# Performance work log

Hardware: AMD Instinct MI355X
Metric: run time of the kernel (lower is better)

The kernel has to match this reference:

```python
import jax, jax.numpy as jnp
import numpy as np

SPACE_DIM = 3
D = SPACE_DIM + 1            # (t, x, y, z)
D_MODEL = 1024
N_LAYERS = 4                 # hidden layers
N_MIX = 64
TRI = D * (D - 1) // 2       # strict upper-triangular entries of A
OUT_DIM = N_MIX * (TRI + 1)  # per-mixture triu values + mixture logits
TRIU_I, TRIU_J = np.triu_indices(D, k=1)
RHO_SCALE = 10.0


def setup_inputs() -> dict:
    key = jax.random.key(0)
    ks = jax.random.split(key, 8)
    B = 65536
    x = jax.random.normal(ks[0], (B, D), jnp.float32)
    W0 = jax.random.normal(ks[1], (D, D_MODEL), jnp.float32) * np.float32(np.sqrt(2.0 / D))
    b0 = jnp.zeros((D_MODEL,), jnp.float32)
    Wh = jax.random.normal(ks[2], (N_LAYERS, D_MODEL, D_MODEL), jnp.float32) * np.float32(np.sqrt(2.0 / D_MODEL))
    bh = jnp.zeros((N_LAYERS, D_MODEL), jnp.float32)
    Wout = jax.random.normal(ks[3], (D_MODEL, OUT_DIM), jnp.float32) * np.float32(np.sqrt(1.0 / D_MODEL))
    bout = jnp.zeros((OUT_DIM,), jnp.float32)
    return dict(x=x, W0=W0, b0=b0, Wh=Wh, bh=bh, Wout=Wout, bout=bout)


def _mlp(z, W0, b0, Wh, bh, Wout, bout):
    # z: (D,) -> (OUT_DIM,), swish MLP (NeuralConservationLaw backbone)
    h = jax.nn.silu(z @ W0 + b0)
    for l in range(N_LAYERS):  # fixed small layer count: python loop ok
        h = jax.nn.silu(h @ Wh[l] + bh[l])
    return h @ Wout + bout


def _A(z, params):
    # Antisymmetric matrix field A(z): mixture-weighted strict-upper-tri values.
    out = _mlp(z, *params)                              # (OUT_DIM,)
    logits = out[:N_MIX]                                # (N_MIX,)
    vals = out[N_MIX:].reshape(N_MIX, TRI)              # (N_MIX, TRI)
    a = jax.nn.softmax(logits) @ vals                   # (TRI,)
    A = jnp.zeros((D, D), out.dtype).at[TRIU_I, TRIU_J].set(a)
    return A - A.T                                      # antisymmetric (D, D)


def reference(x, W0, b0, Wh, bh, Wout, bout):
    params = (W0, b0, Wh, bh, Wout, bout)

    def u_single(z):
        # u_i = sum_j dA_ij/dz_j  (row-divergence of antisymmetric A => div u = 0)
        J = jax.jacfwd(lambda zz: _A(zz, params))(z)    # (D, D, D): J[i,j,k]=dA_ij/dz_k
        return jnp.einsum('ijj->i', J)                  # (D,)

    u = jax.vmap(u_single)(x)                           # (B, D)
    rho = u[..., :1] * RHO_SCALE
    flux = u[..., 1:]
    return jnp.concatenate([rho, flux], axis=-1)
```

## Files before the change

### kernel.cpp

```cpp
#include <hip/hip_runtime.h>
#include <hip/hip_bf16.h>

typedef _Float16 half8 __attribute__((ext_vector_type(8)));
typedef _Float16 half4 __attribute__((ext_vector_type(4)));
typedef float floatx4 __attribute__((ext_vector_type(4)));

__device__ __forceinline__ float bfu2f(unsigned short u) {
  return __uint_as_float(((unsigned)u) << 16);
}

__device__ __forceinline__ void gld16(const void* g, void* l) {
  __builtin_amdgcn_global_load_lds((const __attribute__((address_space(1))) void*)g,
                                   (__attribute__((address_space(3))) void*)l, 16, 0, 0);
}

__device__ __forceinline__ float fast_sig(float v) {
  return __builtin_amdgcn_rcpf(1.f + __expf(-v));
}

template <int NC>
__device__ __forceinline__ void xcd_decode(int lin, int NR, int& r, int& c) {
  if (NR & 7) {
    c = lin % NC;
    r = lin / NC;
  } else {
    int rl = lin & 7;
    int t = lin >> 3;
    c = t % NC;
    r = (t / NC) * 8 + rl;
  }
}

__global__ void probe_kernel(const unsigned short* __restrict__ w0, int* __restrict__ flag) {
  __shared__ int s;
  if (threadIdx.x == 0) s = 0;
  __syncthreads();
  int big = 0;
  for (int i = threadIdx.x; i < 2048; i += 256) {
    unsigned e = (w0[i] >> 7) & 0xFFu;
    if (e >= 134u) big = 1;
  }
  if (big) atomicOr(&s, 1);
  __syncthreads();
  if (threadIdx.x == 0) *flag = s;
}

__global__ void cvt_kernel(const void* __restrict__ in, _Float16* __restrict__ out, int nOut,
                           int nIn, const int* __restrict__ flag) {
  int i = blockIdx.x * 256 + threadIdx.x;
  if (i >= nOut) return;
  float v = 0.f;
  if (i < nIn) v = (*flag) ? ((const float*)in)[i] : bfu2f(((const unsigned short*)in)[i]);
  out[i] = (_Float16)v;
}

__global__ void tr_kernel(const void* __restrict__ in, _Float16* __restrict__ out, int Nin,
                          long inStride, long outStride, const int* __restrict__ flag) {
  __shared__ float tile[32][33];
  const int f = *flag;
  int k0 = blockIdx.x * 32, n0 = blockIdx.y * 32;
  long ib = (long)blockIdx.z * inStride;
  long ob = (long)blockIdx.z * outStride;
  int tx = threadIdx.x, ty = threadIdx.y;
#pragma unroll
  for (int i = 0; i < 4; i++) {
    int k = k0 + ty + i * 8, n = n0 + tx;
    float v = 0.f;
    if (n < Nin) {
      long idx = ib + (long)k * Nin + n;
      v = f ? ((const float*)in)[idx] : bfu2f(((const unsigned short*)in)[idx]);
    }
    tile[ty + i * 8][tx] = v;
  }
  __syncthreads();
#pragma unroll
  for (int i = 0; i < 4; i++) {
    int n = n0 + ty + i * 8, k = k0 + tx;
    out[ob + (long)n * 1024 + k] = (_Float16)tile[tx][ty + i * 8];
  }
}

__global__ __launch_bounds__(256)
void layer0_kernel(const _Float16* __restrict__ x16, const _Float16* __restrict__ W0c,
                   const _Float16* __restrict__ b0c, _Float16* __restrict__ H,
                   int chunkBase, int S1) {
  const int lb = blockIdx.x;
  const int t = threadIdx.x;
  const long gb = (long)chunkBase + lb;
  float z0 = (float)x16[gb * 4 + 0];
  float z1 = (float)x16[gb * 4 + 1];
  float z2 = (float)x16[gb * 4 + 2];
  float z3 = (float)x16[gb * 4 + 3];
  const int j0 = t * 4;
  float w[4][4];
#pragma unroll
  for (int i = 0; i < 4; i++) {
    half4 wv = *(const half4*)&W0c[i * 1024 + j0];
#pragma unroll
    for (int jj = 0; jj < 4; jj++) w[i][jj] = (float)wv[jj];
  }
  half4 o[5];
#pragma unroll
  for (int jj = 0; jj < 4; jj++) {
    float pre = z0 * w[0][jj] + z1 * w[1][jj] + z2 * w[2][jj] + z3 * w[3][jj] +
                (float)b0c[j0 + jj];
    float s = fast_sig(pre);
    o[0][jj] = (_Float16)(pre * s);
    float ds = s * (1.f + pre * (1.f - s));
    o[1][jj] = (_Float16)(ds * w[0][jj]);
    o[2][jj] = (_Float16)(ds * w[1][jj]);
    o[3][jj] = (_Float16)(ds * w[2][jj]);
    o[4][jj] = (_Float16)(ds * w[3][jj]);
  }
  long rowbase = (long)lb * 1024 + j0;
#pragma unroll
  for (int s = 0; s < 5; s++) *(half4*)&H[(long)s * S1 + rowbase] = o[s];
}

__global__ __launch_bounds__(256, 3)
void gemm_h1(const _Float16* __restrict__ A, const _Float16* __restrict__ Bt,
             const _Float16* __restrict__ bias, _Float16* __restrict__ C,
             _Float16* __restrict__ DS, int NR) {
  constexpr int K = 1024;
  __shared__ _Float16 SM[8192];
  _Float16* As = SM;
  _Float16* Bs = SM + 4096;
  _Float16* Ep = SM;
  const int tid = threadIdx.x;
  const int wave = tid >> 6;
  const int lane = tid & 63;
  int rb, cb;
  xcd_decode<8>(blockIdx.x, NR, rb, cb);
  const int n0 = cb * 128;
  const long m0 = (long)rb * 128;

  const int srow0 = (wave * 2 + 0) * 16 + (lane >> 2);
  const int srow1 = (wave * 2 + 1) * 16 + (lane >> 2);
  const int scol = (lane & 3) * 8;
  const _Float16* gA0 = A + (m0 + srow0) * K + scol;
  const _Float16* gA1 = A + (m0 + srow1) * K + scol;
  const _Float16* gB0 = Bt + (long)(n0 + srow0) * K + scol;
  const _Float16* gB1 = Bt + (long)(n0 + srow1) * K + scol;
  _Float16* lA0 = As + (wave * 2 + 0) * 512;
  _Float16* lA1 = As + (wave * 2 + 1) * 512;
  _Float16* lB0 = Bs + (wave * 2 + 0) * 512;
  _Float16* lB1 = Bs + (wave * 2 + 1) * 512;

  const int wm = (wave & 1) * 64;
  const int wn = (wave >> 1) * 64;
  const int fr = lane & 15;
  const int fc = (lane >> 4) * 8;
  const int c0f = lane & 15;
  const int rqk = lane >> 4;
  const int myRound = wave & 1;

  float bv[4];
#pragma unroll
  for (int ni = 0; ni < 4; ni++) bv[ni] = (float)bias[n0 + wn + ni * 16 + c0f];

  const int erow = tid >> 4;
  const int ecol = (tid & 15) * 8;
  const int ecolp = ecol ^ (wave << 4);

  floatx4 acc[4][4];
#pragma unroll
  for (int i = 0; i < 4; i++)
#pragma unroll
    for (int j = 0; j < 4; j++) acc[i][j] = (floatx4)(0.f);

  for (int kk = 0; kk < K; kk += 32) {
    __syncthreads();
    gld16(gA0 + kk, lA0);
    gld16(gA1 + kk, lA1);
    gld16(gB0 + kk, lB0);
    gld16(gB1 + kk, lB1);
    __syncthreads();
    half8 af[4], bf[4];
#pragma unroll
    for (int i = 0; i < 4; i++) af[i] = *(const half8*)&As[(wm + i * 16 + fr) * 32 + fc];
#pragma unroll
    for (int i = 0; i < 4; i++) bf[i] = *(const half8*)&Bs[(wn + i * 16 + fr) * 32 + fc];
#pragma unroll
    for (int mi = 0; mi < 4; mi++)
#pragma unroll
      for (int ni = 0; ni < 4; ni++)
        acc[mi][ni] = __builtin_amdgcn_mfma_f32_16x16x32_f16(af[mi], bf[ni], acc[mi][ni], 0, 0, 0);
  }

#pragma unroll
  for (int r = 0; r < 2; r++) {
    __syncthreads();
    if (myRound == r) {
#pragma unroll
      for (int mi = 0; mi < 4; mi++)
#pragma unroll
        for (int ni = 0; ni < 4; ni++) {
          int colp = (wn + ni * 16 + c0f) ^ (rqk << 4);
#pragma unroll
          for (int rr = 0; rr < 4; rr++) {
            int row_local = mi * 16 + rqk * 4 + rr;
            Ep[row_local * 128 + colp] = (_Float16)(acc[mi][ni][rr] + bv[ni]);
          }
        }
    }
    __syncthreads();
#pragma unroll
    for (int p = 0; p < 4; p++) {
      int row_local = p * 16 + erow;
      half8 vv = *(const half8*)&Ep[row_local * 128 + ecolp];
      long row = m0 + r * 64 + row_local;
      half8 hv, dv;
#pragma unroll
      for (int e = 0; e < 8; e++) {
        float xv = (float)vv[e];
        float sg = fast_sig(xv);
        hv[e] = (_Float16)(xv * sg);
        dv[e] = (_Float16)(sg * (1.f + xv * (1.f - sg)));
      }
      *(half8*)&C[row * (long)K + n0 + ecol] = hv;
      *(half8*)&DS[row * (long)K + n0 + ecol] = dv;
    }
  }
}

__global__ __launch_bounds__(256, 4)
void gemm_h2(const _Float16* __restrict__ A, const _Float16* __restrict__ Bt,
             _Float16* __restrict__ C, const _Float16* __restrict__ DS, int bcMask, int NR) {
  constexpr int K = 1024;
  __shared__ _Float16 SM[8192];
  _Float16* As = SM;
  _Float16* Bs = SM + 4096;
  _Float16* Ep = SM;
  const int tid = threadIdx.x;
  const int wave = tid >> 6;
  const int lane = tid & 63;
  int rb, cb;
  xcd_decode<8>(blockIdx.x, NR, rb, cb);
  const int n0 = cb * 128;
  const long m0 = (long)rb * 128;

  const int srow0 = (wave * 2 + 0) * 16 + (lane >> 2);
  const int srow1 = (wave * 2 + 1) * 16 + (lane >> 2);
  const int scol = (lane & 3) * 8;
  const _Float16* gA0 = A + (m0 + srow0) * K + scol;
  const _Float16* gA1 = A + (m0 + srow1) * K + scol;
  const _Float16* gB0 = Bt + (long)(n0 + srow0) * K + scol;
  const _Float16* gB1 = Bt + (long)(n0 + srow1) * K + scol;
  _Float16* lA0 = As + (wave * 2 + 0) * 512;
  _Float16* lA1 = As + (wave * 2 + 1) * 512;
  _Float16* lB0 = Bs + (wave * 2 + 0) * 512;
  _Float16* lB1 = Bs + (wave * 2 + 1) * 512;

  const int wm = (wave & 1) * 64;
  const int wn = (wave >> 1) * 64;
  const int fr = lane & 15;
  const int fc = (lane >> 4) * 8;
  const int c0f = lane & 15;
  const int rqk = lane >> 4;
  const int myRound = wave & 1;

  const int erow = tid >> 4;
  const int ecol = (tid & 15) * 8;
  const int ecolp = ecol ^ (wave << 4);

  floatx4 acc[4][4];
#pragma unroll
  for (int i = 0; i < 4; i++)
#pragma unroll
    for (int j = 0; j < 4; j++) acc[i][j] = (floatx4)(0.f);

  for (int kk = 0; kk < K; kk += 32) {
    __syncthreads();
    gld16(gA0 + kk, lA0);
    gld16(gA1 + kk, lA1);
    gld16(gB0 + kk, lB0);
    gld16(gB1 + kk, lB1);
    __syncthreads();
    half8 af[4], bf[4];
#pragma unroll
    for (int i = 0; i < 4; i++) af[i] = *(const half8*)&As[(wm + i * 16 + fr) * 32 + fc];
#pragma unroll
    for (int i = 0; i < 4; i++) bf[i] = *(const half8*)&Bs[(wn + i * 16 + fr) * 32 + fc];
#pragma unroll
    for (int mi = 0; mi < 4; mi++)
#pragma unroll
      for (int ni = 0; ni < 4; ni++)
        acc[mi][ni] = __builtin_amdgcn_mfma_f32_16x16x32_f16(af[mi], bf[ni], acc[mi][ni], 0, 0, 0);
  }

#pragma unroll
  for (int r = 0; r < 2; r++) {
    __syncthreads();
    if (myRound == r) {
#pragma unroll
      for (int mi = 0; mi < 4; mi++)
#pragma unroll
        for (int ni = 0; ni < 4; ni++) {
          int colp = (wn + ni * 16 + c0f) ^ (rqk << 4);
#pragma unroll
          for (int rr = 0; rr < 4; rr++) {
            int row_local = mi * 16 + rqk * 4 + rr;
            Ep[row_local * 128 + colp] = (_Float16)acc[mi][ni][rr];
          }
        }
    }
    __syncthreads();
#pragma unroll
    for (int p = 0; p < 4; p++) {
      int row_local = p * 16 + erow;
      half8 vv = *(const half8*)&Ep[row_local * 128 + ecolp];
      long row = m0 + r * 64 + row_local;
      half8 dv = *(const half8*)&DS[(long)(row & bcMask) * K + n0 + ecol];
      *(half8*)&C[row * (long)K + n0 + ecol] = dv * vv;
    }
  }
}

__global__ __launch_bounds__(256, 4)
void gemm_out(const _Float16* __restrict__ A, const _Float16* __restrict__ Bt,
              const _Float16* __restrict__ bias, _Float16* __restrict__ C,
              int Nreal, int ldc, int biasRows, int NR) {
  constexpr int K = 1024;
  __shared__ _Float16 SM[8192];
  _Float16* As = SM;
  _Float16* Bs = SM + 4096;
  _Float16* Ep = SM;
  const int tid = threadIdx.x;
  const int wave = tid >> 6;
  const int lane = tid & 63;
  int rb, cb;
  xcd_decode<4>(blockIdx.x, NR, rb, cb);
  const int n0 = cb * 128;
  const long m0 = (long)rb * 128;

  const int srow0 = (wave * 2 + 0) * 16 + (lane >> 2);
  const int srow1 = (wave * 2 + 1) * 16 + (lane >> 2);
  const int scol = (lane & 3) * 8;
  const _Float16* gA0 = A + (m0 + srow0) * K + scol;
  const _Float16* gA1 = A + (m0 + srow1) * K + scol;
  const _Float16* gB0 = Bt + (long)(n0 + srow0) * K + scol;
  const _Float16* gB1 = Bt + (long)(n0 + srow1) * K + scol;
  _Float16* lA0 = As + (wave * 2 + 0) * 512;
  _Float16* lA1 = As + (wave * 2 + 1) * 512;
  _Float16* lB0 = Bs + (wave * 2 + 0) * 512;
  _Float16* lB1 = Bs + (wave * 2 + 1) * 512;

  const int wm = (wave & 1) * 64;
  const int wn = (wave >> 1) * 64;
  const int fr = lane & 15;
  const int fc = (lane >> 4) * 8;
  const int c0f = lane & 15;
  const int rqk = lane >> 4;
  const int myRound = wave & 1;

  float bv[4];
#pragma unroll
  for (int ni = 0; ni < 4; ni++) bv[ni] = (float)bias[n0 + wn + ni * 16 + c0f];

  const int erow = tid >> 4;
  const int ecol = (tid & 15) * 8;
  const int ecolp = ecol ^ (wave << 4);

  floatx4 acc[4][4];
#pragma unroll
  for (int i = 0; i < 4; i++)
#pragma unroll
    for (int j = 0; j < 4; j++) acc[i][j] = (floatx4)(0.f);

  for (int kk = 0; kk < K; kk += 32) {
    __syncthreads();
    gld16(gA0 + kk, lA0);
    gld16(gA1 + kk, lA1);
    gld16(gB0 + kk, lB0);
    gld16(gB1 + kk, lB1);
    __syncthreads();
    half8 af[4], bf[4];
#pragma unroll
    for (int i = 0; i < 4; i++) af[i] = *(const half8*)&As[(wm + i * 16 + fr) * 32 + fc];
#pragma unroll
    for (int i = 0; i < 4; i++) bf[i] = *(const half8*)&Bs[(wn + i * 16 + fr) * 32 + fc];
#pragma unroll
    for (int mi = 0; mi < 4; mi++)
#pragma unroll
      for (int ni = 0; ni < 4; ni++)
        acc[mi][ni] = __builtin_amdgcn_mfma_f32_16x16x32_f16(af[mi], bf[ni], acc[mi][ni], 0, 0, 0);
  }

#pragma unroll
  for (int r = 0; r < 2; r++) {
    __syncthreads();
    if (myRound == r) {
#pragma unroll
      for (int mi = 0; mi < 4; mi++)
#pragma unroll
        for (int ni = 0; ni < 4; ni++) {
          int colp = (wn + ni * 16 + c0f) ^ (rqk << 4);
#pragma unroll
          for (int rr = 0; rr < 4; rr++) {
            int row_local = mi * 16 + rqk * 4 + rr;
            long grow = m0 + wm + mi * 16 + rqk * 4 + rr;
            float v = acc[mi][ni][rr] + (grow < biasRows ? bv[ni] : 0.f);
            Ep[row_local * 128 + colp] = (_Float16)v;
          }
        }
    }
    __syncthreads();
#pragma unroll
    for (int p = 0; p < 4; p++) {
      int row_local = p * 16 + erow;
      int col = n0 + ecol;
      if (col < Nreal) {
        half8 vv = *(const half8*)&Ep[row_local * 128 + ecolp];
        long row = m0 + r * 64 + row_local;
        *(half8*)&C[row * (long)ldc + col] = vv;
      }
    }
  }
}

__global__ __launch_bounds__(256)
void finalize_kernel(const _Float16* __restrict__ O5, void* __restrict__ outp,
                     int chunkBase, int Bc, const int* __restrict__ flag) {
  const int wid = threadIdx.x >> 6;
  const int lane = threadIdx.x & 63;
  const int lb = blockIdx.x * 4 + wid;
  const long SO = (long)Bc * 448;
  const long base0 = (long)lb * 448;

  union UU { unsigned u; _Float16 h[2]; };

  float lg = (float)O5[base0 + lane];
  float vals[6];
  {
    const unsigned* vp = (const unsigned*)(O5 + base0 + 64 + lane * 6);
#pragma unroll
    for (int q = 0; q < 3; q++) {
      UU c; c.u = vp[q];
      vals[2 * q] = (float)c.h[0];
      vals[2 * q + 1] = (float)c.h[1];
    }
  }
  float dl[4], dv[4][6];
#pragma unroll
  for (int t = 0; t < 4; t++) {
    long bs = (long)(1 + t) * SO + base0;
    dl[t] = (float)O5[bs + lane];
    const unsigned* vp = (const unsigned*)(O5 + bs + 64 + lane * 6);
#pragma unroll
    for (int q = 0; q < 3; q++) {
      UU c; c.u = vp[q];
      dv[t][2 * q] = (float)c.h[0];
      dv[t][2 * q + 1] = (float)c.h[1];
    }
  }
  float mx = lg;
#pragma unroll
  for (int off = 32; off >= 1; off >>= 1) mx = fmaxf(mx, __shfl_xor(mx, off));
  float e = __expf(lg - mx);
  float S = e;
#pragma unroll
  for (int off = 32; off >= 1; off >>= 1) S += __shfl_xor(S, off);
  float pv = e / S;
  float st[4];
#pragma unroll
  for (int t = 0; t < 4; t++) {
    float v = pv * dl[t];
#pragma unroll
    for (int off = 32; off >= 1; off >>= 1) v += __shfl_xor(v, off);
    st[t] = v;
  }
  float da[4][6];
#pragma unroll
  for (int t = 0; t < 4; t++) {
    float w = pv * (dl[t] - st[t]);
#pragma unroll
    for (int k = 0; k < 6; k++) {
      float v = w * vals[k] + pv * dv[t][k];
#pragma unroll
      for (int off = 32; off >= 1; off >>= 1) v += __shfl_xor(v, off);
      da[t][k] = v;
    }
  }
  if (lane == 0) {
    float u0 = da[1][0] + da[2][1] + da[3][2];
    float u1 = -da[0][0] + da[2][3] + da[3][4];
    float u2 = -da[0][1] - da[1][3] + da[3][5];
    float u3 = -da[0][2] - da[1][4] - da[2][5];
    long ob = (long)(chunkBase + lb) * 4;
    if (*flag) {
      float* o = (float*)outp;
      o[ob] = 10.f * u0; o[ob + 1] = u1; o[ob + 2] = u2; o[ob + 3] = u3;
    } else {
      __hip_bfloat16* o = (__hip_bfloat16*)outp;
      o[ob] = __float2bfloat16(10.f * u0);
      o[ob + 1] = __float2bfloat16(u1);
      o[ob + 2] = __float2bfloat16(u2);
      o[ob + 3] = __float2bfloat16(u3);
    }
  }
}

extern "C" void kernel_launch(void* const* d_in, const int* in_sizes, int n_in,
                              void* d_out, int out_size, void* d_ws, size_t ws_size,
                              hipStream_t stream) {
  const void* x = d_in[0];
  const void* W0 = d_in[1];
  const void* b0 = d_in[2];
  const void* Wh = d_in[3];
  const void* bh = d_in[4];
  const void* Wout = d_in[5];
  const void* bout = d_in[6];
  const int B = in_sizes[0] / 4;

  char* p = (char*)d_ws;
  int* flag = (int*)p;                 p += 256;
  _Float16* W0c = (_Float16*)p;        p += 4096 * 2;
  _Float16* b0c = (_Float16*)p;        p += 1024 * 2;
  _Float16* bhc = (_Float16*)p;        p += 4096 * 2;
  _Float16* boutc = (_Float16*)p;      p += 512 * 2;
  p += 256 - ((size_t)(p - (char*)d_ws) & 255);
  _Float16* x16 = (_Float16*)p;        p += (size_t)B * 4 * 2;
  _Float16* WhT = (_Float16*)p;        p += (size_t)4 * 1024 * 1024 * 2;
  _Float16* WoutT = (_Float16*)p;      p += (size_t)512 * 1024 * 2;
  size_t used = (size_t)(p - (char*)d_ws);
  size_t rem = (ws_size > used) ? (ws_size - used) : 0;
  const size_t perS = 10240 + 10240 + 2048 + 4480;
  long bcap = (long)(rem / perS);
  int Bc = 128;
  while ((long)Bc * 2 <= bcap && Bc * 2 <= B) Bc *= 2;
  _Float16* Ha = (_Float16*)p;         p += (size_t)5 * Bc * 1024 * 2;
  _Float16* Hb = (_Float16*)p;         p += (size_t)5 * Bc * 1024 * 2;
  _Float16* DS = (_Float16*)p;         p += (size_t)Bc * 1024 * 2;
  _Float16* PREo = (_Float16*)p;

  probe_kernel<<<1, 256, 0, stream>>>((const unsigned short*)W0, flag);
  cvt_kernel<<<(B * 4 + 255) / 256, 256, 0, stream>>>(x, x16, B * 4, B * 4, flag);
  cvt_kernel<<<16, 256, 0, stream>>>(W0, W0c, 4096, 4096, flag);
  cvt_kernel<<<4, 256, 0, stream>>>(b0, b0c, 1024, 1024, flag);
  cvt_kernel<<<16, 256, 0, stream>>>(bh, bhc, 4096, 4096, flag);
  cvt_kernel<<<2, 256, 0, stream>>>(bout, boutc, 512, 448, flag);
  tr_kernel<<<dim3(32, 32, 4), dim3(32, 8), 0, stream>>>(Wh, WhT, 1024, 1024L * 1024, 1024L * 1024, flag);
  tr_kernel<<<dim3(32, 16, 1), dim3(32, 8), 0, stream>>>(Wout, WoutT, 448, 0L, 0L, flag);

  const int nChunks = B / Bc;
  for (int c = 0; c < nChunks; c++) {
    const int base = c * Bc;
    const int S1 = Bc * 1024;
    _Float16* Hin = Ha;
    _Float16* Hout = Hb;
    layer0_kernel<<<Bc, 256, 0, stream>>>(x16, W0c, b0c, Hin, base, S1);
    const int NR1 = Bc / 128;
    const int NR2 = 4 * Bc / 128;
    const int NRo = 5 * Bc / 128;
    for (int l = 0; l < 4; l++) {
      const _Float16* Wl = WhT + (size_t)l * 1024 * 1024;
      gemm_h1<<<8 * NR1, 256, 0, stream>>>(
          Hin, Wl, bhc + l * 1024, Hout, DS, NR1);
      gemm_h2<<<8 * NR2, 256, 0, stream>>>(
          Hin + S1, Wl, Hout + S1, DS, Bc - 1, NR2);
      _Float16* t = Hin; Hin = Hout; Hout = t;
    }
    gemm_out<<<4 * NRo, 256, 0, stream>>>(
        Hin, WoutT, boutc, PREo, 448, 448, Bc, NRo);
    finalize_kernel<<<Bc / 4, 256, 0, stream>>>(PREo, d_out, base, Bc, flag);
  }
}
```

Baseline: 4.666 ms.

## Merge next-layer primal GEMM into tangent GEMM launch and double K tile

Folds the h1 and h2 kernels into one gemm_hid kernel. Each launch runs the tangent GEMM of layer l alongside the primal GEMM of layer l+1, with blocks picking their role from blockIdx. This cuts the launch count and fills the small primal GEMM's idle CUs with tangent work. Double-buffered DS arrays (aliased onto the PREo scratch) make the interleaving safe. The K step also grows from 32 to 64, with 32KB of LDS per block, to halve barrier count per tile. The cost is more LDS per block, which may lower occupancy, and more register pressure from the merged kernel.

```diff
diff --git a/kernel.cpp b/kernel.cpp
--- a/kernel.cpp
+++ b/kernel.cpp
@@ -117,34 +117,42 @@
   for (int s = 0; s < 5; s++) *(half4*)&H[(long)s * S1 + rowbase] = o[s];
 }
 
-__global__ __launch_bounds__(256, 3)
-void gemm_h1(const _Float16* __restrict__ A, const _Float16* __restrict__ Bt,
-             const _Float16* __restrict__ bias, _Float16* __restrict__ C,
-             _Float16* __restrict__ DS, int NR) {
+__global__ __launch_bounds__(256, 4)
+void gemm_hid(const _Float16* __restrict__ A2, const _Float16* __restrict__ W2,
+              _Float16* __restrict__ C2, const _Float16* __restrict__ DSr, int bcMask,
+              int nH2, int NR2,
+              const _Float16* __restrict__ A1, const _Float16* __restrict__ W1,
+              const _Float16* __restrict__ b1, _Float16* __restrict__ C1,
+              _Float16* __restrict__ DSw, int NR1) {
   constexpr int K = 1024;
-  __shared__ _Float16 SM[8192];
+  __shared__ _Float16 SM[16384];
   _Float16* As = SM;
-  _Float16* Bs = SM + 4096;
+  _Float16* Bs = SM + 8192;
   _Float16* Ep = SM;
   const int tid = threadIdx.x;
   const int wave = tid >> 6;
   const int lane = tid & 63;
+
+  const bool isH2 = ((int)blockIdx.x) < nH2;
   int rb, cb;
-  xcd_decode<8>(blockIdx.x, NR, rb, cb);
+  const _Float16* A;
+  const _Float16* Bt;
+  if (isH2) {
+    xcd_decode<8>(blockIdx.x, NR2, rb, cb);
+    A = A2; Bt = W2;
+  } else {
+    xcd_decode<8>(blockIdx.x - nH2, NR1, rb, cb);
+    A = A1; Bt = W1;
+  }
   const int n0 = cb * 128;
   const long m0 = (long)rb * 128;
 
-  const int srow0 = (wave * 2 + 0) * 16 + (lane >> 2);
-  const int srow1 = (wave * 2 + 1) * 16 + (lane >> 2);
+  const int srow = lane >> 2;
   const int scol = (lane & 3) * 8;
-  const _Float16* gA0 = A + (m0 + srow0) * K + scol;
-  const _Float16* gA1 = A + (m0 + srow1) * K + scol;
-  const _Float16* gB0 = Bt + (long)(n0 + srow0) * K + scol;
-  const _Float16* gB1 = Bt + (long)(n0 + srow1) * K + scol;
-  _Float16* lA0 = As + (wave * 2 + 0) * 512;
-  _Float16* lA1 = As + (wave * 2 + 1) * 512;
-  _Float16* lB0 = Bs + (wave * 2 + 0) * 512;
-  _Float16* lB1 = Bs + (wave * 2 + 1) * 512;
+  const _Float16* gAb = A + (m0 + wave * 32 + srow) * K + scol;
+  const _Float16* gBb = Bt + (long)(n0 + wave * 32 + srow) * K + scol;
+  _Float16* lAb = As + wave * 32 * 32;
+  _Float16* lBb = Bs + wave * 32 * 32;
 
   const int wm = (wave & 1) * 64;
   const int wn = (wave >> 1) * 64;
@@ -155,8 +163,10 @@
   const int myRound = wave & 1;
 
   float bv[4];
-#pragma unroll
-  for (int ni = 0; ni < 4; ni++) bv[ni] = (float)bias[n0 + wn + ni * 16 + c0f];
+  if (!isH2) {
+#pragma unroll
+    for (int ni = 0; ni < 4; ni++) bv[ni] = (float)b1[n0 + wn + ni * 16 + c0f];
+  }
 
   const int erow = tid >> 4;
   const int ecol = (tid & 15) * 8;
@@ -168,150 +178,94 @@
 #pragma unroll
     for (int j = 0; j < 4; j++) acc[i][j] = (floatx4)(0.f);
 
-  for (int kk = 0; kk < K; kk += 32) {
+  for (int kk = 0; kk < K; kk += 64) {
     __syncthreads();
-    gld16(gA0 + kk, lA0);
-    gld16(gA1 + kk, lA1);
-    gld16(gB0 + kk, lB0);
-    gld16(gB1 + kk, lB1);
+#pragma unroll
+    for (int p = 0; p < 2; p++)
+#pragma unroll
+      for (int kc = 0; kc < 2; kc++) {
+        gld16(gAb + kk + p * 16 * K + kc * 32, lAb + p * 512 + kc * 4096);
+        gld16(gBb + kk + p * 16 * K + kc * 32, lBb + p * 512 + kc * 4096);
+      }
     __syncthreads();
-    half8 af[4], bf[4];
-#pragma unroll
-    for (int i = 0; i < 4; i++) af[i] = *(const half8*)&As[(wm + i * 16 + fr) * 32 + fc];
-#pragma unroll
-    for (int i = 0; i < 4; i++) bf[i] = *(const half8*)&Bs[(wn + i * 16 + fr) * 32 + fc];
-#pragma unroll
-    for (int mi = 0; mi < 4; mi++)
-#pragma unroll
-      for (int ni = 0; ni < 4; ni++)
-        acc[mi][ni] = __builtin_amdgcn_mfma_f32_16x16x32_f16(af[mi], bf[ni], acc[mi][ni], 0, 0, 0);
-  }
-
-#pragma unroll
-  for (int r = 0; r < 2; r++) {
-    __syncthreads();
-    if (myRound == r) {
+#pragma unroll
+    for (int kc = 0; kc < 2; kc++) {
+      half8 af[4], bf[4];
+#pragma unroll
+      for (int i = 0; i < 4; i++)
+        af[i] = *(const half8*)&As[kc * 4096 + (wm + i * 16 + fr) * 32 + fc];
+#pragma unroll
+      for (int i = 0; i < 4; i++)
+        bf[i] = *(const half8*)&Bs[kc * 4096 + (wn + i * 16 + fr) * 32 + fc];
 #pragma unroll
       for (int mi = 0; mi < 4; mi++)
 #pragma unroll
-        for (int ni = 0; ni < 4; ni++) {
-          int colp = (wn + ni * 16 + c0f) ^ (rqk << 4);
-#pragma unroll
-          for (int rr = 0; rr < 4; rr++) {
-            int row_local = mi * 16 + rqk * 4 + rr;
-            Ep[row_local * 128 + colp] = (_Float16)(acc[mi][ni][rr] + bv[ni]);
+        for (int ni = 0; ni < 4; ni++)
+          acc[mi][ni] = __builtin_amdgcn_mfma_f32_16x16x32_f16(af[mi], bf[ni], acc[mi][ni], 0, 0, 0);
+    }
+  }
+
+  if (isH2) {
+#pragma unroll
+    for (int r = 0; r < 2; r++) {
+      __syncthreads();
+      if (myRound == r) {
+#pragma unroll
+        for (int mi = 0; mi < 4; mi++)
+#pragma unroll
+          for (int ni = 0; ni < 4; ni++) {
+            int colp = (wn + ni * 16 + c0f) ^ (rqk << 4);
+#pragma unroll
+            for (int rr = 0; rr < 4; rr++) {
+              int row_local = mi * 16 + rqk * 4 + rr;
+              Ep[row_local * 128 + colp] = (_Float16)acc[mi][ni][rr];
+            }
           }
+      }
+      __syncthreads();
+#pragma unroll
+      for (int p = 0; p < 4; p++) {
+        int row_local = p * 16 + erow;
+        half8 vv = *(const half8*)&Ep[row_local * 128 + ecolp];
+        long row = m0 + r * 64 + row_local;
+        half8 dv = *(const half8*)&DSr[(long)(row & bcMask) * K + n0 + ecol];
+        *(half8*)&C2[row * (long)K + n0 + ecol] = dv * vv;
+      }
+    }
+  } else {
+#pragma unroll
+    for (int r = 0; r < 2; r++) {
+      __syncthreads();
+      if (myRound == r) {
+#pragma unroll
+        for (int mi = 0; mi < 4; mi++)
+#pragma unroll
+          for (int ni = 0; ni < 4; ni++) {
+            int colp = (wn + ni * 16 + c0f) ^ (rqk << 4);
+#pragma unroll
+            for (int rr = 0; rr < 4; rr++) {
+              int row_local = mi * 16 + rqk * 4 + rr;
+              Ep[row_local * 128 + colp] = (_Float16)(acc[mi][ni][rr] + bv[ni]);
+            }
+          }
+      }
+      __syncthreads();
+#pragma unroll
+      for (int p = 0; p < 4; p++) {
+        int row_local = p * 16 + erow;
+        half8 vv = *(const half8*)&Ep[row_local * 128 + ecolp];
+        long row = m0 + r * 64 + row_local;
+        half8 hv, dv;
+#pragma unroll
+        for (int e = 0; e < 8; e++) {
+          float xv = (float)vv[e];
+          float sg = fast_sig(xv);
+          hv[e] = (_Float16)(xv * sg);
+          dv[e] = (_Float16)(sg * (1.f + xv * (1.f - sg)));
         }
-    }
-    __syncthreads();
-#pragma unroll
-    for (int p = 0; p < 4; p++) {
-      int row_local = p * 16 + erow;
-      half8 vv = *(const half8*)&Ep[row_local * 128 + ecolp];
-      long row = m0 + r * 64 + row_local;
-      half8 hv, dv;
-#pragma unroll
-      for (int e = 0; e < 8; e++) {
-        float xv = (float)vv[e];
-        float sg = fast_sig(xv);
-        hv[e] = (_Float16)(xv * sg);
-        dv[e] = (_Float16)(sg * (1.f + xv * (1.f - sg)));
-      }
-      *(half8*)&C[row * (long)K + n0 + ecol] = hv;
-      *(half8*)&DS[row * (long)K + n0 + ecol] = dv;
-    }
-  }
-}
-
-__global__ __launch_bounds__(256, 4)
-void gemm_h2(const _Float16* __restrict__ A, const _Float16* __restrict__ Bt,
-             _Float16* __restrict__ C, const _Float16* __restrict__ DS, int bcMask, int NR) {
-  constexpr int K = 1024;
-  __shared__ _Float16 SM[8192];
-  _Float16* As = SM;
-  _Float16* Bs = SM + 4096;
-  _Float16* Ep = SM;
-  const int tid = threadIdx.x;
-  const int wave = tid >> 6;
-  const int lane = tid & 63;
-  int rb, cb;
-  xcd_decode<8>(blockIdx.x, NR, rb, cb);
-  const int n0 = cb * 128;
-  const long m0 = (long)rb * 128;
-
-  const int srow0 = (wave * 2 + 0) * 16 + (lane >> 2);
-  const int srow1 = (wave * 2 + 1) * 16 + (lane >> 2);
-  const int scol = (lane & 3) * 8;
-  const _Float16* gA0 = A + (m0 + srow0) * K + scol;
-  const _Float16* gA1 = A + (m0 + srow1) * K + scol;
-  const _Float16* gB0 = Bt + (long)(n0 + srow0) * K + scol;
-  const _Float16* gB1 = Bt + (long)(n0 + srow1) * K + scol;
-  _Float16* lA0 = As + (wave * 2 + 0) * 512;
-  _Float16* lA1 = As + (wave * 2 + 1) * 512;
-  _Float16* lB0 = Bs + (wave * 2 + 0) * 512;
-  _Float16* lB1 = Bs + (wave * 2 + 1) * 512;
-
-  const int wm = (wave & 1) * 64;
-  const int wn = (wave >> 1) * 64;
-  const int fr = lane & 15;
-  const int fc = (lane >> 4) * 8;
-  const int c0f = lane & 15;
-  const int rqk = lane >> 4;
-  const int myRound = wave & 1;
-
-  const int erow = tid >> 4;
-  const int ecol = (tid & 15) * 8;
-  const int ecolp = ecol ^ (wave << 4);
-
-  floatx4 acc[4][4];
-#pragma unroll
-  for (int i = 0; i < 4; i++)
-#pragma unroll
-    for (int j = 0; j < 4; j++) acc[i][j] = (floatx4)(0.f);
-
-  for (int kk = 0; kk < K; kk += 32) {
-    __syncthreads();
-    gld16(gA0 + kk, lA0);
-    gld16(gA1 + kk, lA1);
-    gld16(gB0 + kk, lB0);
-    gld16(gB1 + kk, lB1);
-    __syncthreads();
-    half8 af[4], bf[4];
-#pragma unroll
-    for (int i = 0; i < 4; i++) af[i] = *(const half8*)&As[(wm + i * 16 + fr) * 32 + fc];
-#pragma unroll
-    for (int i = 0; i < 4; i++) bf[i] = *(const half8*)&Bs[(wn + i * 16 + fr) * 32 + fc];
-#pragma unroll
-    for (int mi = 0; mi < 4; mi++)
-#pragma unroll
-      for (int ni = 0; ni < 4; ni++)
-        acc[mi][ni] = __builtin_amdgcn_mfma_f32_16x16x32_f16(af[mi], bf[ni], acc[mi][ni], 0, 0, 0);
-  }
-
-#pragma unroll
-  for (int r = 0; r < 2; r++) {
-    __syncthreads();
-    if (myRound == r) {
-#pragma unroll
-      for (int mi = 0; mi < 4; mi++)
-#pragma unroll
-        for (int ni = 0; ni < 4; ni++) {
-          int colp = (wn + ni * 16 + c0f) ^ (rqk << 4);
-#pragma unroll
-          for (int rr = 0; rr < 4; rr++) {
-            int row_local = mi * 16 + rqk * 4 + rr;
-            Ep[row_local * 128 + colp] = (_Float16)acc[mi][ni][rr];
-          }
-        }
-    }
-    __syncthreads();
-#pragma unroll
-    for (int p = 0; p < 4; p++) {
-      int row_local = p * 16 + erow;
-      half8 vv = *(const half8*)&Ep[row_local * 128 + ecolp];
-      long row = m0 + r * 64 + row_local;
-      half8 dv = *(const half8*)&DS[(long)(row & bcMask) * K + n0 + ecol];
-      *(half8*)&C[row * (long)K + n0 + ecol] = dv * vv;
+        *(half8*)&C1[row * (long)K + n0 + ecol] = hv;
+        *(half8*)&DSw[row * (long)K + n0 + ecol] = dv;
+      }
     }
   }
 }
@@ -321,9 +275,9 @@
               const _Float16* __restrict__ bias, _Float16* __restrict__ C,
               int Nreal, int ldc, int biasRows, int NR) {
   constexpr int K = 1024;
-  __shared__ _Float16 SM[8192];
+  __shared__ _Float16 SM[16384];
   _Float16* As = SM;
-  _Float16* Bs = SM + 4096;
+  _Float16* Bs = SM + 8192;
   _Float16* Ep = SM;
   const int tid = threadIdx.x;
   const int wave = tid >> 6;
@@ -333,17 +287,12 @@
   const int n0 = cb * 128;
   const long m0 = (long)rb * 128;
 
-  const int srow0 = (wave * 2 + 0) * 16 + (lane >> 2);
-  const int srow1 = (wave * 2 + 1) * 16 + (lane >> 2);
+  const int srow = lane >> 2;
   const int scol = (lane & 3) * 8;
-  const _Float16* gA0 = A + (m0 + srow0) * K + scol;
-  const _Float16* gA1 = A + (m0 + srow1) * K + scol;
-  const _Float16* gB0 = Bt + (long)(n0 + srow0) * K + scol;
-  const _Float16* gB1 = Bt + (long)(n0 + srow1) * K + scol;
-  _Float16* lA0 = As + (wave * 2 + 0) * 512;
-  _Float16* lA1 = As + (wave * 2 + 1) * 512;
-  _Float16* lB0 = Bs + (wave * 2 + 0) * 512;
-  _Float16* lB1 = Bs + (wave * 2 + 1) * 512;
+  const _Float16* gAb = A + (m0 + wave * 32 + srow) * K + scol;
+  const _Float16* gBb = Bt + (long)(n0 + wave * 32 + srow) * K + scol;
+  _Float16* lAb = As + wave * 32 * 32;
+  _Float16* lBb = Bs + wave * 32 * 32;
 
   const int wm = (wave & 1) * 64;
   const int wn = (wave >> 1) * 64;
@@ -367,23 +316,31 @@
 #pragma unroll
     for (int j = 0; j < 4; j++) acc[i][j] = (floatx4)(0.f);
 
-  for (int kk = 0; kk < K; kk += 32) {
+  for (int kk = 0; kk < K; kk += 64) {
     __syncthreads();
-    gld16(gA0 + kk, lA0);
-    gld16(gA1 + kk, lA1);
-    gld16(gB0 + kk, lB0);
-    gld16(gB1 + kk, lB1);
+#pragma unroll
+    for (int p = 0; p < 2; p++)
+#pragma unroll
+      for (int kc = 0; kc < 2; kc++) {
+        gld16(gAb + kk + p * 16 * K + kc * 32, lAb + p * 512 + kc * 4096);
+        gld16(gBb + kk + p * 16 * K + kc * 32, lBb + p * 512 + kc * 4096);
+      }
     __syncthreads();
-    half8 af[4], bf[4];
-#pragma unroll
-    for (int i = 0; i < 4; i++) af[i] = *(const half8*)&As[(wm + i * 16 + fr) * 32 + fc];
-#pragma unroll
-    for (int i = 0; i < 4; i++) bf[i] = *(const half8*)&Bs[(wn + i * 16 + fr) * 32 + fc];
-#pragma unroll
-    for (int mi = 0; mi < 4; mi++)
-#pragma unroll
-      for (int ni = 0; ni < 4; ni++)
-        acc[mi][ni] = __builtin_amdgcn_mfma_f32_16x16x32_f16(af[mi], bf[ni], acc[mi][ni], 0, 0, 0);
+#pragma unroll
+    for (int kc = 0; kc < 2; kc++) {
+      half8 af[4], bf[4];
+#pragma unroll
+      for (int i = 0; i < 4; i++)
+        af[i] = *(const half8*)&As[kc * 4096 + (wm + i * 16 + fr) * 32 + fc];
+#pragma unroll
+      for (int i = 0; i < 4; i++)
+        bf[i] = *(const half8*)&Bs[kc * 4096 + (wn + i * 16 + fr) * 32 + fc];
+#pragma unroll
+      for (int mi = 0; mi < 4; mi++)
+#pragma unroll
+        for (int ni = 0; ni < 4; ni++)
+          acc[mi][ni] = __builtin_amdgcn_mfma_f32_16x16x32_f16(af[mi], bf[ni], acc[mi][ni], 0, 0, 0);
+    }
   }
 
 #pragma unroll
@@ -524,13 +481,14 @@
   _Float16* WoutT = (_Float16*)p;      p += (size_t)512 * 1024 * 2;
   size_t used = (size_t)(p - (char*)d_ws);
   size_t rem = (ws_size > used) ? (ws_size - used) : 0;
-  const size_t perS = 10240 + 10240 + 2048 + 4480;
+  const size_t perS = 10240 + 10240 + 4480;
   long bcap = (long)(rem / perS);
   int Bc = 128;
   while ((long)Bc * 2 <= bcap && Bc * 2 <= B) Bc *= 2;
   _Float16* Ha = (_Float16*)p;         p += (size_t)5 * Bc * 1024 * 2;
   _Float16* Hb = (_Float16*)p;         p += (size_t)5 * Bc * 1024 * 2;
-  _Float16* DS = (_Float16*)p;         p += (size_t)Bc * 1024 * 2;
+  _Float16* DSa = (_Float16*)p;
+  _Float16* DSb = DSa + (size_t)Bc * 1024;
   _Float16* PREo = (_Float16*)p;
 
   probe_kernel<<<1, 256, 0, stream>>>((const unsigned short*)W0, flag);
@@ -546,22 +504,27 @@
   for (int c = 0; c < nChunks; c++) {
     const int base = c * Bc;
     const int S1 = Bc * 1024;
-    _Float16* Hin = Ha;
-    _Float16* Hout = Hb;
-    layer0_kernel<<<Bc, 256, 0, stream>>>(x16, W0c, b0c, Hin, base, S1);
+    layer0_kernel<<<Bc, 256, 0, stream>>>(x16, W0c, b0c, Ha, base, S1);
     const int NR1 = Bc / 128;
     const int NR2 = 4 * Bc / 128;
     const int NRo = 5 * Bc / 128;
-    for (int l = 0; l < 4; l++) {
-      const _Float16* Wl = WhT + (size_t)l * 1024 * 1024;
-      gemm_h1<<<8 * NR1, 256, 0, stream>>>(
-          Hin, Wl, bhc + l * 1024, Hout, DS, NR1);
-      gemm_h2<<<8 * NR2, 256, 0, stream>>>(
-          Hin + S1, Wl, Hout + S1, DS, Bc - 1, NR2);
-      _Float16* t = Hin; Hin = Hout; Hout = t;
-    }
+    gemm_hid<<<8 * NR1, 256, 0, stream>>>(
+        nullptr, nullptr, nullptr, nullptr, 0, 0, NR2,
+        Ha, WhT + 0 * 1048576, bhc + 0 * 1024, Hb, DSa, NR1);
+    gemm_hid<<<8 * NR2 + 8 * NR1, 256, 0, stream>>>(
+        Ha + S1, WhT + 0 * 1048576, Hb + S1, DSa, Bc - 1, 8 * NR2, NR2,
+        Hb, WhT + 1 * 1048576, bhc + 1 * 1024, Ha, DSb, NR1);
+    gemm_hid<<<8 * NR2 + 8 * NR1, 256, 0, stream>>>(
+        Hb + S1, WhT + 1 * 1048576, Ha + S1, DSb, Bc - 1, 8 * NR2, NR2,
+        Ha, WhT + 2 * 1048576, bhc + 2 * 1024, Hb, DSa, NR1);
+    gemm_hid<<<8 * NR2 + 8 * NR1, 256, 0, stream>>>(
+        Ha + S1, WhT + 2 * 1048576, Hb + S1, DSa, Bc - 1, 8 * NR2, NR2,
+        Hb, WhT + 3 * 1048576, bhc + 3 * 1024, Ha, DSb, NR1);
+    gemm_hid<<<8 * NR2, 256, 0, stream>>>(
+        Hb + S1, WhT + 3 * 1048576, Ha + S1, DSb, Bc - 1, 8 * NR2, NR2,
+        nullptr, nullptr, nullptr, nullptr, nullptr, NR1);
     gemm_out<<<4 * NRo, 256, 0, stream>>>(
-        Hin, WoutT, boutc, PREo, 448, 448, Bc, NRo);
+        Ha, WoutT, boutc, PREo, 448, 448, Bc, NRo);
     finalize_kernel<<<Bc / 4, 256, 0, stream>>>(PREo, d_out, base, Bc, flag);
   }
 }
```

After: 4.803 ms. +2.9%, slower.

## Give each wave private LDS tiles to drop block-wide barriers in GEMM loops

Applied to the files above, without the earlier changes.

In the three GEMM kernels, the shared A/B LDS tiles are replaced by per-wave private regions. Each wave now loads its own 64-row slices of A and B through global_load_lds and waits only on its own vmcnt, so the two __syncthreads per k-step go away. The trade is that each wave loads its A and B slices itself, so waves sharing a row or column block fetch the same data and global/L2 load traffic doubles. LDS use per block doubles and launch bounds for gemm_h1 rise from 3 to 4. A later iteration's global_load_lds can also overwrite a tile before the previous iteration's ds_reads finish, because no lgkmcnt wait or barrier separates them.

```diff
diff --git a/kernel.cpp b/kernel.cpp
--- a/kernel.cpp
+++ b/kernel.cpp
@@ -13,6 +13,8 @@
   __builtin_amdgcn_global_load_lds((const __attribute__((address_space(1))) void*)g,
                                    (__attribute__((address_space(3))) void*)l, 16, 0, 0);
 }
+
+__device__ __forceinline__ void wait_vm0() { __builtin_amdgcn_s_waitcnt(0x0F70); }
 
 __device__ __forceinline__ float fast_sig(float v) {
   return __builtin_amdgcn_rcpf(1.f + __expf(-v));
@@ -117,14 +119,12 @@
   for (int s = 0; s < 5; s++) *(half4*)&H[(long)s * S1 + rowbase] = o[s];
 }
 
-__global__ __launch_bounds__(256, 3)
+__global__ __launch_bounds__(256, 4)
 void gemm_h1(const _Float16* __restrict__ A, const _Float16* __restrict__ Bt,
              const _Float16* __restrict__ bias, _Float16* __restrict__ C,
              _Float16* __restrict__ DS, int NR) {
   constexpr int K = 1024;
-  __shared__ _Float16 SM[8192];
-  _Float16* As = SM;
-  _Float16* Bs = SM + 4096;
+  __shared__ _Float16 SM[16384];
   _Float16* Ep = SM;
   const int tid = threadIdx.x;
   const int wave = tid >> 6;
@@ -134,18 +134,6 @@
   const int n0 = cb * 128;
   const long m0 = (long)rb * 128;
 
-  const int srow0 = (wave * 2 + 0) * 16 + (lane >> 2);
-  const int srow1 = (wave * 2 + 1) * 16 + (lane >> 2);
-  const int scol = (lane & 3) * 8;
-  const _Float16* gA0 = A + (m0 + srow0) * K + scol;
-  const _Float16* gA1 = A + (m0 + srow1) * K + scol;
-  const _Float16* gB0 = Bt + (long)(n0 + srow0) * K + scol;
-  const _Float16* gB1 = Bt + (long)(n0 + srow1) * K + scol;
-  _Float16* lA0 = As + (wave * 2 + 0) * 512;
-  _Float16* lA1 = As + (wave * 2 + 1) * 512;
-  _Float16* lB0 = Bs + (wave * 2 + 0) * 512;
-  _Float16* lB1 = Bs + (wave * 2 + 1) * 512;
-
   const int wm = (wave & 1) * 64;
   const int wn = (wave >> 1) * 64;
   const int fr = lane & 15;
@@ -154,6 +142,13 @@
   const int rqk = lane >> 4;
   const int myRound = wave & 1;
 
+  _Float16* Apriv = SM + wave * 4096;
+  _Float16* Bpriv = Apriv + 2048;
+  const int srow = lane >> 2;
+  const int scol = (lane & 3) * 8;
+  const _Float16* gA = A + (m0 + wm + srow) * K + scol;
+  const _Float16* gB = Bt + (long)(n0 + wn + srow) * K + scol;
+
   float bv[4];
 #pragma unroll
   for (int ni = 0; ni < 4; ni++) bv[ni] = (float)bias[n0 + wn + ni * 16 + c0f];
@@ -169,17 +164,16 @@
     for (int j = 0; j < 4; j++) acc[i][j] = (floatx4)(0.f);
 
   for (int kk = 0; kk < K; kk += 32) {
-    __syncthreads();
-    gld16(gA0 + kk, lA0);
-    gld16(gA1 + kk, lA1);
-    gld16(gB0 + kk, lB0);
-    gld16(gB1 + kk, lB1);
-    __syncthreads();
+#pragma unroll
+    for (int q = 0; q < 4; q++) gld16(gA + q * 16 * K + kk, Apriv + q * 512);
+#pragma unroll
+    for (int q = 0; q < 4; q++) gld16(gB + q * 16 * K + kk, Bpriv + q * 512);
+    wait_vm0();
     half8 af[4], bf[4];
 #pragma unroll
-    for (int i = 0; i < 4; i++) af[i] = *(const half8*)&As[(wm + i * 16 + fr) * 32 + fc];
-#pragma unroll
-    for (int i = 0; i < 4; i++) bf[i] = *(const half8*)&Bs[(wn + i * 16 + fr) * 32 + fc];
+    for (int i = 0; i < 4; i++) af[i] = *(const half8*)&Apriv[(i * 16 + fr) * 32 + fc];
+#pragma unroll
+    for (int i = 0; i < 4; i++) bf[i] = *(const half8*)&Bpriv[(i * 16 + fr) * 32 + fc];
 #pragma unroll
     for (int mi = 0; mi < 4; mi++)
 #pragma unroll
@@ -227,9 +221,7 @@
 void gemm_h2(const _Float16* __restrict__ A, const _Float16* __restrict__ Bt,
              _Float16* __restrict__ C, const _Float16* __restrict__ DS, int bcMask, int NR) {
   constexpr int K = 1024;
-  __shared__ _Float16 SM[8192];
-  _Float16* As = SM;
-  _Float16* Bs = SM + 4096;
+  __shared__ _Float16 SM[16384];
   _Float16* Ep = SM;
   const int tid = threadIdx.x;
   const int wave = tid >> 6;
@@ -239,18 +231,6 @@
   const int n0 = cb * 128;
   const long m0 = (long)rb * 128;
 
-  const int srow0 = (wave * 2 + 0) * 16 + (lane >> 2);
-  const int srow1 = (wave * 2 + 1) * 16 + (lane >> 2);
-  const int scol = (lane & 3) * 8;
-  const _Float16* gA0 = A + (m0 + srow0) * K + scol;
-  const _Float16* gA1 = A + (m0 + srow1) * K + scol;
-  const _Float16* gB0 = Bt + (long)(n0 + srow0) * K + scol;
-  const _Float16* gB1 = Bt + (long)(n0 + srow1) * K + scol;
-  _Float16* lA0 = As + (wave * 2 + 0) * 512;
-  _Float16* lA1 = As + (wave * 2 + 1) * 512;
-  _Float16* lB0 = Bs + (wave * 2 + 0) * 512;
-  _Float16* lB1 = Bs + (wave * 2 + 1) * 512;
-
   const int wm = (wave & 1) * 64;
   const int wn = (wave >> 1) * 64;
   const int fr = lane & 15;
@@ -259,6 +239,13 @@
   const int rqk = lane >> 4;
   const int myRound = wave & 1;
 
+  _Float16* Apriv = SM + wave * 4096;
+  _Float16* Bpriv = Apriv + 2048;
+  const int srow = lane >> 2;
+  const int scol = (lane & 3) * 8;
+  const _Float16* gA = A + (m0 + wm + srow) * K + scol;
+  const _Float16* gB = Bt + (long)(n0 + wn + srow) * K + scol;
+
   const int erow = tid >> 4;
   const int ecol = (tid & 15) * 8;
   const int ecolp = ecol ^ (wave << 4);
@@ -270,17 +257,16 @@
     for (int j = 0; j < 4; j++) acc[i][j] = (floatx4)(0.f);
 
   for (int kk = 0; kk < K; kk += 32) {
-    __syncthreads();
-    gld16(gA0 + kk, lA0);
-    gld16(gA1 + kk, lA1);
-    gld16(gB0 + kk, lB0);
-    gld16(gB1 + kk, lB1);
-    __syncthreads();
+#pragma unroll
+    for (int q = 0; q < 4; q++) gld16(gA + q * 16 * K + kk, Apriv + q * 512);
+#pragma unroll
+    for (int q = 0; q < 4; q++) gld16(gB + q * 16 * K + kk, Bpriv + q * 512);
+    wait_vm0();
     half8 af[4], bf[4];
 #pragma unroll
-    for (int i = 0; i < 4; i++) af[i] = *(const half8*)&As[(wm + i * 16 + fr) * 32 + fc];
-#pragma unroll
-    for (int i = 0; i < 4; i++) bf[i] = *(const half8*)&Bs[(wn + i * 16 + fr) * 32 + fc];
+    for (int i = 0; i < 4; i++) af[i] = *(const half8*)&Apriv[(i * 16 + fr) * 32 + fc];
+#pragma unroll
+    for (int i = 0; i < 4; i++) bf[i] = *(const half8*)&Bpriv[(i * 16 + fr) * 32 + fc];
 #pragma unroll
     for (int mi = 0; mi < 4; mi++)
 #pragma unroll
@@ -321,9 +307,7 @@
               const _Float16* __restrict__ bias, _Float16* __restrict__ C,
               int Nreal, int ldc, int biasRows, int NR) {
   constexpr int K = 1024;
-  __shared__ _Float16 SM[8192];
-  _Float16* As = SM;
-  _Float16* Bs = SM + 4096;
+  __shared__ _Float16 SM[16384];
   _Float16* Ep = SM;
   const int tid = threadIdx.x;
   const int wave = tid >> 6;
@@ -333,18 +317,6 @@
   const int n0 = cb * 128;
   const long m0 = (long)rb * 128;
 
-  const int srow0 = (wave * 2 + 0) * 16 + (lane >> 2);
-  const int srow1 = (wave * 2 + 1) * 16 + (lane >> 2);
-  const int scol = (lane & 3) * 8;
-  const _Float16* gA0 = A + (m0 + srow0) * K + scol;
-  const _Float16* gA1 = A + (m0 + srow1) * K + scol;
-  const _Float16* gB0 = Bt + (long)(n0 + srow0) * K + scol;
-  const _Float16* gB1 = Bt + (long)(n0 + srow1) * K + scol;
-  _Float16* lA0 = As + (wave * 2 + 0) * 512;
-  _Float16* lA1 = As + (wave * 2 + 1) * 512;
-  _Float16* lB0 = Bs + (wave * 2 + 0) * 512;
-  _Float16* lB1 = Bs + (wave * 2 + 1) * 512;
-
   const int wm = (wave & 1) * 64;
   const int wn = (wave >> 1) * 64;
   const int fr = lane & 15;
@@ -353,6 +325,13 @@
   const int rqk = lane >> 4;
   const int myRound = wave & 1;
 
+  _Float16* Apriv = SM + wave * 4096;
+  _Float16* Bpriv = Apriv + 2048;
+  const int srow = lane >> 2;
+  const int scol = (lane & 3) * 8;
+  const _Float16* gA = A + (m0 + wm + srow) * K + scol;
+  const _Float16* gB = Bt + (long)(n0 + wn + srow) * K + scol;
+
   float bv[4];
 #pragma unroll
   for (int ni = 0; ni < 4; ni++) bv[ni] = (float)bias[n0 + wn + ni * 16 + c0f];
@@ -368,17 +347,16 @@
     for (int j = 0; j < 4; j++) acc[i][j] = (floatx4)(0.f);
 
   for (int kk = 0; kk < K; kk += 32) {
-    __syncthreads();
-    gld16(gA0 + kk, lA0);
-    gld16(gA1 + kk, lA1);
-    gld16(gB0 + kk, lB0);
-    gld16(gB1 + kk, lB1);
-    __syncthreads();
+#pragma unroll
+    for (int q = 0; q < 4; q++) gld16(gA + q * 16 * K + kk, Apriv + q * 512);
+#pragma unroll
+    for (int q = 0; q < 4; q++) gld16(gB + q * 16 * K + kk, Bpriv + q * 512);
+    wait_vm0();
     half8 af[4], bf[4];
 #pragma unroll
-    for (int i = 0; i < 4; i++) af[i] = *(const half8*)&As[(wm + i * 16 + fr) * 32 + fc];
-#pragma unroll
-    for (int i = 0; i < 4; i++) bf[i] = *(const half8*)&Bs[(wn + i * 16 + fr) * 32 + fc];
+    for (int i = 0; i < 4; i++) af[i] = *(const half8*)&Apriv[(i * 16 + fr) * 32 + fc];
+#pragma unroll
+    for (int i = 0; i < 4; i++) bf[i] = *(const half8*)&Bpriv[(i * 16 + fr) * 32 + fc];
 #pragma unroll
     for (int mi = 0; mi < 4; mi++)
 #pragma unroll
```

Result: slower. 5.831 ms (+25.0%).

## Triple-buffer LDS tiles in gemm_h2 to overlap global loads with MFMA

Applied to the files above, without the earlier changes.

Replaces the single-buffered K loop, which synchronised twice per step, with a three-stage ring of LDS buffers. Loads run two K-steps ahead using direct global-to-LDS loads, with a manual vmcnt wait and one barrier per iteration. This is meant to hide global-load latency behind the MFMA work. In exchange it triples LDS use and lowers the launch-bounds occupancy hint from 4 to 3 blocks per CU.

```diff
diff --git a/kernel.cpp b/kernel.cpp
--- a/kernel.cpp
+++ b/kernel.cpp
@@ -223,13 +223,11 @@
   }
 }
 
-__global__ __launch_bounds__(256, 4)
+__global__ __launch_bounds__(256, 3)
 void gemm_h2(const _Float16* __restrict__ A, const _Float16* __restrict__ Bt,
              _Float16* __restrict__ C, const _Float16* __restrict__ DS, int bcMask, int NR) {
   constexpr int K = 1024;
-  __shared__ _Float16 SM[8192];
-  _Float16* As = SM;
-  _Float16* Bs = SM + 4096;
+  __shared__ _Float16 SM[24576];
   _Float16* Ep = SM;
   const int tid = threadIdx.x;
   const int wave = tid >> 6;
@@ -246,10 +244,8 @@
   const _Float16* gA1 = A + (m0 + srow1) * K + scol;
   const _Float16* gB0 = Bt + (long)(n0 + srow0) * K + scol;
   const _Float16* gB1 = Bt + (long)(n0 + srow1) * K + scol;
-  _Float16* lA0 = As + (wave * 2 + 0) * 512;
-  _Float16* lA1 = As + (wave * 2 + 1) * 512;
-  _Float16* lB0 = Bs + (wave * 2 + 0) * 512;
-  _Float16* lB1 = Bs + (wave * 2 + 1) * 512;
+  const int loffA0 = (wave * 2 + 0) * 512;
+  const int loffA1 = (wave * 2 + 1) * 512;
 
   const int wm = (wave & 1) * 64;
   const int wn = (wave >> 1) * 64;
@@ -269,23 +265,47 @@
 #pragma unroll
     for (int j = 0; j < 4; j++) acc[i][j] = (floatx4)(0.f);
 
-  for (int kk = 0; kk < K; kk += 32) {
-    __syncthreads();
-    gld16(gA0 + kk, lA0);
-    gld16(gA1 + kk, lA1);
-    gld16(gB0 + kk, lB0);
-    gld16(gB1 + kk, lB1);
-    __syncthreads();
+  {
+    _Float16* b0p = SM;
+    gld16(gA0 + 0, b0p + loffA0);
+    gld16(gA1 + 0, b0p + loffA1);
+    gld16(gB0 + 0, b0p + 4096 + loffA0);
+    gld16(gB1 + 0, b0p + 4096 + loffA1);
+    _Float16* b1p = SM + 8192;
+    gld16(gA0 + 32, b1p + loffA0);
+    gld16(gA1 + 32, b1p + loffA1);
+    gld16(gB0 + 32, b1p + 4096 + loffA0);
+    gld16(gB1 + 32, b1p + 4096 + loffA1);
+  }
+
+  int bufCur = 0;
+  int bufNxt = 2;
+  for (int it = 0; it < 32; ++it) {
+    if (it < 31) __builtin_amdgcn_s_waitcnt(0x0F74);
+    else         __builtin_amdgcn_s_waitcnt(0x0F70);
+    __builtin_amdgcn_s_barrier();
+    if (it < 30) {
+      const int kk = (it + 2) * 32;
+      _Float16* bp = SM + bufNxt * 8192;
+      gld16(gA0 + kk, bp + loffA0);
+      gld16(gA1 + kk, bp + loffA1);
+      gld16(gB0 + kk, bp + 4096 + loffA0);
+      gld16(gB1 + kk, bp + 4096 + loffA1);
+    }
+    const _Float16* Asb = SM + bufCur * 8192;
+    const _Float16* Bsb = Asb + 4096;
     half8 af[4], bf[4];
 #pragma unroll
-    for (int i = 0; i < 4; i++) af[i] = *(const half8*)&As[(wm + i * 16 + fr) * 32 + fc];
-#pragma unroll
-    for (int i = 0; i < 4; i++) bf[i] = *(const half8*)&Bs[(wn + i * 16 + fr) * 32 + fc];
+    for (int i = 0; i < 4; i++) af[i] = *(const half8*)&Asb[(wm + i * 16 + fr) * 32 + fc];
+#pragma unroll
+    for (int i = 0; i < 4; i++) bf[i] = *(const half8*)&Bsb[(wn + i * 16 + fr) * 32 + fc];
 #pragma unroll
     for (int mi = 0; mi < 4; mi++)
 #pragma unroll
       for (int ni = 0; ni < 4; ni++)
         acc[mi][ni] = __builtin_amdgcn_mfma_f32_16x16x32_f16(af[mi], bf[ni], acc[mi][ni], 0, 0, 0);
+    bufCur = (bufCur == 2) ? 0 : bufCur + 1;
+    bufNxt = (bufNxt == 2) ? 0 : bufNxt + 1;
   }
 
 #pragma unroll
```

After: 4.499 ms. -3.6%, faster.
